# Kernel tuning notes

Measured on AMD Instinct MI355X. Metric: run time of the kernel, lower is better.

## Reference

```python
import jax, jax.numpy as jnp
import numpy as np

N = 1048576
BINS = 32
HID = 64
OUT = 64
IN_DIMS = 7


def setup_inputs() -> dict:
    key = jax.random.key(0)
    ks = jax.random.split(key, 9)
    pos01 = jax.random.uniform(ks[0], (N, 3), dtype=jnp.float32)
    wi01 = jax.random.uniform(ks[1], (N, 3), dtype=jnp.float32)
    rough01 = jax.random.uniform(ks[2], (N, 1), dtype=jnp.float32)
    enc_dim = IN_DIMS * BINS  # 224
    W1 = jax.random.normal(ks[3], (enc_dim, HID), dtype=jnp.float32) / np.sqrt(enc_dim)
    b1 = jnp.zeros((HID,), dtype=jnp.float32)
    W2 = jax.random.normal(ks[4], (HID, HID), dtype=jnp.float32) / np.sqrt(HID)
    b2 = jnp.zeros((HID,), dtype=jnp.float32)
    W3 = jax.random.normal(ks[5], (HID, OUT), dtype=jnp.float32) / np.sqrt(HID)
    b3 = jnp.zeros((OUT,), dtype=jnp.float32)
    centers = jnp.linspace(0.0, 1.0, BINS, dtype=jnp.float32)
    return {"pos01": pos01, "wi01": wi01, "rough01": rough01,
            "W1": W1, "b1": b1, "W2": W2, "b2": b2, "W3": W3, "b3": b3,
            "centers": centers}


def reference(pos01, wi01, rough01, W1, b1, W2, b2, W3, b3, centers):
    # Concatenate + clamp to [0,1]: [N, 7]
    x = jnp.clip(jnp.concatenate([pos01, wi01, rough01], axis=1), 0.0, 1.0)
    sigma = 1.0 / BINS
    # OneBlob gaussian encoding: [N, 7, BINS] -> [N, 7*BINS]
    diff = x[:, :, None] - centers[None, None, :]
    enc = jnp.exp(-0.5 * (diff / sigma) ** 2).reshape(x.shape[0], -1)
    # 3-layer MLP with ReLU
    h = jax.nn.relu(enc @ W1 + b1)
    h = jax.nn.relu(h @ W2 + b2)
    return h @ W3 + b3
```

## Files before the change

kernel.cpp:

```cpp
#include <hip/hip_runtime.h>

typedef __bf16 bf16x8 __attribute__((ext_vector_type(8)));
typedef float  f32x4  __attribute__((ext_vector_type(4)));

constexpr int HID = 64;
constexpr float K1   = 27.178297f;
constexpr float STEP = -K1 / 31.0f;


__global__ void prep_kernel(const float* __restrict__ W1,
                            const float* __restrict__ W2,
                            const float* __restrict__ W3,
                            bf16x8* __restrict__ ws)
{
    const int f = blockIdx.x;
    const int l = threadIdx.x;
    const int g = l >> 4, r = l & 15;
    bf16x8 v;
    if (f < 28) {
        const int kk = f >> 2, mt = f & 3;
#pragma unroll
        for (int j = 0; j < 8; ++j)
            v[j] = (__bf16)W1[(32 * kk + 8 * g + j) * HID + 16 * mt + r];
    } else {
        const float* W = (f < 36) ? W2 : W3;
        const int fi = (f < 36) ? (f - 28) : (f - 36);
        const int mt = fi >> 1, kk2 = fi & 1;
#pragma unroll
        for (int j = 0; j < 8; ++j) {
            const int k = 32 * kk2 + 16 * (j >> 2) + 4 * g + (j & 3);
            v[j] = (__bf16)W[k * HID + 16 * mt + r];
        }
    }
    ws[f * 64 + l] = v;
}

__device__ __forceinline__ void load_x(const float* __restrict__ pos,
                                       const float* __restrict__ wi,
                                       const float* __restrict__ rough,
                                       int row, float* x)
{
    x[0] = pos[row * 3 + 0]; x[1] = pos[row * 3 + 1]; x[2] = pos[row * 3 + 2];
    x[3] = wi[row * 3 + 0];  x[4] = wi[row * 3 + 1];  x[5] = wi[row * 3 + 2];
    x[6] = rough[row];
}

__global__ __launch_bounds__(256, 3)
void cond_net_kernel(const float* __restrict__ pos, const float* __restrict__ wi,
                     const float* __restrict__ rough,
                     const float* __restrict__ b1, const float* __restrict__ b2,
                     const float* __restrict__ b3,
                     const bf16x8* __restrict__ ws,
                     float* __restrict__ out)
{
    __shared__ __align__(16) char lds[44 * 1024 + 768];

    const int tid = threadIdx.x;
    const int l = tid & 63, wv = tid >> 6, g = l >> 4, r = l & 15;

#pragma unroll
    for (int i = 0; i < 11; ++i) {
        const int fr = wv * 11 + i;
        __builtin_amdgcn_global_load_lds(
            (const __attribute__((address_space(1))) void*)(ws + fr * 64 + l),
            (__attribute__((address_space(3))) void*)(lds + fr * 1024),
            16, 0, 0);
    }
    if (wv < 3) {
        const float* bp = (wv == 0) ? b1 : (wv == 1) ? b2 : b3;
        __builtin_amdgcn_global_load_lds(
            (const __attribute__((address_space(1))) void*)(bp + l),
            (__attribute__((address_space(3))) void*)(lds + 44 * 1024 + wv * 256),
            4, 0, 0);
    }

    const int rbase = blockIdx.x * 256 + wv * 64 + r;
    float A[4][7];
#pragma unroll
    for (int t = 0; t < 4; ++t) {
        float x[7];
        load_x(pos, wi, rough, rbase + 16 * t, x);
#pragma unroll
        for (int d = 0; d < 7; ++d)
            A[t][d] = fmaf(K1, fminf(fmaxf(x[d], 0.0f), 1.0f), STEP * (float)(8 * g));
    }

    __syncthreads();

    const char* lb = (const char*)lds + l * 16;
    const char* bb = (const char*)lds + 44 * 1024 + g * 16;

    f32x4 acc1[4][4];
    {
        f32x4 b1v[4];
#pragma unroll
        for (int mt = 0; mt < 4; ++mt) b1v[mt] = *(const f32x4*)(bb + mt * 64);
#pragma unroll
        for (int t = 0; t < 4; ++t)
#pragma unroll
            for (int mt = 0; mt < 4; ++mt) acc1[t][mt] = b1v[mt];
    }

#pragma unroll
    for (int kk = 0; kk < 7; ++kk) {
        bf16x8 e[4];
#pragma unroll
        for (int t = 0; t < 4; ++t)
#pragma unroll
            for (int j = 0; j < 8; ++j) {
                const float d = A[t][kk] + (float)j * STEP;
                e[t][j] = (__bf16)__builtin_amdgcn_exp2f(-(d * d));
            }
#pragma unroll
        for (int mt = 0; mt < 4; ++mt) {
            const bf16x8 wf = *(const bf16x8*)(lb + (kk * 4 + mt) * 1024);
#pragma unroll
            for (int t = 0; t < 4; ++t)
                acc1[t][mt] = __builtin_amdgcn_mfma_f32_16x16x32_bf16(wf, e[t], acc1[t][mt], 0, 0, 0);
        }
    }

#pragma unroll
    for (int p = 0; p < 2; ++p) {
        bf16x8 h1f[2][2];
#pragma unroll
        for (int tt = 0; tt < 2; ++tt)
#pragma unroll
            for (int kk2 = 0; kk2 < 2; ++kk2) {
                bf16x8 v;
#pragma unroll
                for (int j = 0; j < 8; ++j)
                    v[j] = (__bf16)fmaxf(acc1[2 * p + tt][2 * kk2 + (j >> 2)][j & 3], 0.0f);
                h1f[tt][kk2] = v;
            }

        f32x4 acc2[2][4];
#pragma unroll
        for (int mt = 0; mt < 4; ++mt) {
            const f32x4 b2v = *(const f32x4*)(bb + 256 + mt * 64);
            acc2[0][mt] = b2v; acc2[1][mt] = b2v;
        }
#pragma unroll
        for (int kk2 = 0; kk2 < 2; ++kk2)
#pragma unroll
            for (int mt = 0; mt < 4; ++mt) {
                const bf16x8 wf = *(const bf16x8*)(lb + (28 + mt * 2 + kk2) * 1024);
#pragma unroll
                for (int tt = 0; tt < 2; ++tt)
                    acc2[tt][mt] = __builtin_amdgcn_mfma_f32_16x16x32_bf16(wf, h1f[tt][kk2], acc2[tt][mt], 0, 0, 0);
            }

        bf16x8 h2f[2][2];
#pragma unroll
        for (int tt = 0; tt < 2; ++tt)
#pragma unroll
            for (int kk2 = 0; kk2 < 2; ++kk2) {
                bf16x8 v;
#pragma unroll
                for (int j = 0; j < 8; ++j)
                    v[j] = (__bf16)fmaxf(acc2[tt][2 * kk2 + (j >> 2)][j & 3], 0.0f);
                h2f[tt][kk2] = v;
            }

        f32x4 acc3[2][4];
#pragma unroll
        for (int mt = 0; mt < 4; ++mt) {
            const f32x4 b3v = *(const f32x4*)(bb + 512 + mt * 64);
            acc3[0][mt] = b3v; acc3[1][mt] = b3v;
        }
#pragma unroll
        for (int kk2 = 0; kk2 < 2; ++kk2)
#pragma unroll
            for (int mt = 0; mt < 4; ++mt) {
                const bf16x8 wf = *(const bf16x8*)(lb + (36 + mt * 2 + kk2) * 1024);
#pragma unroll
                for (int tt = 0; tt < 2; ++tt)
                    acc3[tt][mt] = __builtin_amdgcn_mfma_f32_16x16x32_bf16(wf, h2f[tt][kk2], acc3[tt][mt], 0, 0, 0);
            }

#pragma unroll
        for (int tt = 0; tt < 2; ++tt) {
            const int row = rbase + 16 * (2 * p + tt);
#pragma unroll
            for (int mt = 0; mt < 4; ++mt)
                __builtin_nontemporal_store(acc3[tt][mt],
                    (f32x4*)(out + (size_t)row * 64 + 16 * mt + 4 * g));
        }
    }
}

extern "C" void kernel_launch(void* const* d_in, const int* in_sizes, int n_in,
                              void* d_out, int out_size, void* d_ws, size_t ws_size,
                              hipStream_t stream) {
    const float* pos     = (const float*)d_in[0];
    const float* wi      = (const float*)d_in[1];
    const float* rough   = (const float*)d_in[2];
    const float* W1      = (const float*)d_in[3];
    const float* b1      = (const float*)d_in[4];
    const float* W2      = (const float*)d_in[5];
    const float* b2      = (const float*)d_in[6];
    const float* W3      = (const float*)d_in[7];
    const float* b3      = (const float*)d_in[8];
    float* out = (float*)d_out;

    bf16x8* ws = (bf16x8*)d_ws;

    const int n = in_sizes[0] / 3;
    hipLaunchKernelGGL(prep_kernel, dim3(44), dim3(64), 0, stream, W1, W2, W3, ws);
    hipLaunchKernelGGL(cond_net_kernel, dim3(n / 256), dim3(256), 0, stream,
                       pos, wi, rough, b1, b2, b3, (const bf16x8*)ws, out);
}
```

Measured before the change: 90.23 us.

## Use 512-thread blocks processing 1024 rows in a loop to amortize weight staging

Blocks grow to 512 threads (8 waves) and each wave runs two iterations of 64 rows, so one block covers 1024 rows and the LDS weight load is amortized over four times as many rows. Layers 2 and 3 now process all four row tiles at once instead of in two halves, and input loads move inside the loop. The risks are higher register pressure from the wider acc2/acc3 arrays under launch_bounds(512,4), and fewer blocks in the grid.

After: 92.76 us. 2.8% more time.

```diff
diff --git a/kernel.cpp b/kernel.cpp
--- a/kernel.cpp
+++ b/kernel.cpp
@@ -45,7 +45,7 @@
     x[6] = rough[row];
 }
 
-__global__ __launch_bounds__(256, 3)
+__global__ __launch_bounds__(512, 4)
 void cond_net_kernel(const float* __restrict__ pos, const float* __restrict__ wi,
                      const float* __restrict__ rough,
                      const float* __restrict__ b1, const float* __restrict__ b2,
@@ -58,14 +58,11 @@
     const int tid = threadIdx.x;
     const int l = tid & 63, wv = tid >> 6, g = l >> 4, r = l & 15;
 
-#pragma unroll
-    for (int i = 0; i < 11; ++i) {
-        const int fr = wv * 11 + i;
+    for (int fr = wv; fr < 44; fr += 8)
         __builtin_amdgcn_global_load_lds(
             (const __attribute__((address_space(1))) void*)(ws + fr * 64 + l),
             (__attribute__((address_space(3))) void*)(lds + fr * 1024),
             16, 0, 0);
-    }
     if (wv < 3) {
         const float* bp = (wv == 0) ? b1 : (wv == 1) ? b2 : b3;
         __builtin_amdgcn_global_load_lds(
@@ -74,71 +71,75 @@
             4, 0, 0);
     }
 
-    const int rbase = blockIdx.x * 256 + wv * 64 + r;
-    float A[4][7];
-#pragma unroll
-    for (int t = 0; t < 4; ++t) {
-        float x[7];
-        load_x(pos, wi, rough, rbase + 16 * t, x);
-#pragma unroll
-        for (int d = 0; d < 7; ++d)
-            A[t][d] = fmaf(K1, fminf(fmaxf(x[d], 0.0f), 1.0f), STEP * (float)(8 * g));
-    }
+    const float base_g = STEP * (float)(8 * g);
+    const int rbase = blockIdx.x * 1024 + wv * 64 + r;
 
     __syncthreads();
 
-    const char* lb = (const char*)lds + l * 16;
-    const char* bb = (const char*)lds + 44 * 1024 + g * 16;
-
-    f32x4 acc1[4][4];
-    {
-        f32x4 b1v[4];
-#pragma unroll
-        for (int mt = 0; mt < 4; ++mt) b1v[mt] = *(const f32x4*)(bb + mt * 64);
+    unsigned int ldsoff = 0;
+#pragma unroll 1
+    for (int it = 0; it < 2; ++it) {
+        asm volatile("" : "+v"(ldsoff));
+        const char* lb = (const char*)lds + ldsoff + l * 16;
+        const char* bb = (const char*)lds + ldsoff + 44 * 1024 + g * 16;
+
+        const int row0 = rbase + it * 512;
+
+        float A[4][7];
+#pragma unroll
+        for (int t = 0; t < 4; ++t) {
+            float x[7];
+            load_x(pos, wi, rough, row0 + 16 * t, x);
+#pragma unroll
+            for (int d = 0; d < 7; ++d)
+                A[t][d] = fmaf(K1, fminf(fmaxf(x[d], 0.0f), 1.0f), base_g);
+        }
+
+        f32x4 acc1[4][4];
+#pragma unroll
+        for (int mt = 0; mt < 4; ++mt) {
+            const f32x4 bv = *(const f32x4*)(bb + mt * 64);
+#pragma unroll
+            for (int t = 0; t < 4; ++t) acc1[t][mt] = bv;
+        }
+
+#pragma unroll
+        for (int kk = 0; kk < 7; ++kk) {
+            bf16x8 e[4];
+#pragma unroll
+            for (int t = 0; t < 4; ++t)
+#pragma unroll
+                for (int j = 0; j < 8; ++j) {
+                    const float d = A[t][kk] + (float)j * STEP;
+                    e[t][j] = (__bf16)__builtin_amdgcn_exp2f(-(d * d));
+                }
+#pragma unroll
+            for (int mt = 0; mt < 4; ++mt) {
+                const bf16x8 wf = *(const bf16x8*)(lb + (kk * 4 + mt) * 1024);
+#pragma unroll
+                for (int t = 0; t < 4; ++t)
+                    acc1[t][mt] = __builtin_amdgcn_mfma_f32_16x16x32_bf16(wf, e[t], acc1[t][mt], 0, 0, 0);
+            }
+        }
+
+        bf16x8 h1f[4][2];
 #pragma unroll
         for (int t = 0; t < 4; ++t)
-#pragma unroll
-            for (int mt = 0; mt < 4; ++mt) acc1[t][mt] = b1v[mt];
-    }
-
-#pragma unroll
-    for (int kk = 0; kk < 7; ++kk) {
-        bf16x8 e[4];
-#pragma unroll
-        for (int t = 0; t < 4; ++t)
-#pragma unroll
-            for (int j = 0; j < 8; ++j) {
-                const float d = A[t][kk] + (float)j * STEP;
-                e[t][j] = (__bf16)__builtin_amdgcn_exp2f(-(d * d));
-            }
-#pragma unroll
-        for (int mt = 0; mt < 4; ++mt) {
-            const bf16x8 wf = *(const bf16x8*)(lb + (kk * 4 + mt) * 1024);
-#pragma unroll
-            for (int t = 0; t < 4; ++t)
-                acc1[t][mt] = __builtin_amdgcn_mfma_f32_16x16x32_bf16(wf, e[t], acc1[t][mt], 0, 0, 0);
-        }
-    }
-
-#pragma unroll
-    for (int p = 0; p < 2; ++p) {
-        bf16x8 h1f[2][2];
-#pragma unroll
-        for (int tt = 0; tt < 2; ++tt)
 #pragma unroll
             for (int kk2 = 0; kk2 < 2; ++kk2) {
                 bf16x8 v;
 #pragma unroll
                 for (int j = 0; j < 8; ++j)
-                    v[j] = (__bf16)fmaxf(acc1[2 * p + tt][2 * kk2 + (j >> 2)][j & 3], 0.0f);
-                h1f[tt][kk2] = v;
-            }
-
-        f32x4 acc2[2][4];
+                    v[j] = (__bf16)fmaxf(acc1[t][2 * kk2 + (j >> 2)][j & 3], 0.0f);
+                h1f[t][kk2] = v;
+            }
+
+        f32x4 acc2[4][4];
 #pragma unroll
         for (int mt = 0; mt < 4; ++mt) {
-            const f32x4 b2v = *(const f32x4*)(bb + 256 + mt * 64);
-            acc2[0][mt] = b2v; acc2[1][mt] = b2v;
+            const f32x4 bv = *(const f32x4*)(bb + 256 + mt * 64);
+#pragma unroll
+            for (int t = 0; t < 4; ++t) acc2[t][mt] = bv;
         }
 #pragma unroll
         for (int kk2 = 0; kk2 < 2; ++kk2)
@@ -146,27 +147,28 @@
             for (int mt = 0; mt < 4; ++mt) {
                 const bf16x8 wf = *(const bf16x8*)(lb + (28 + mt * 2 + kk2) * 1024);
 #pragma unroll
-                for (int tt = 0; tt < 2; ++tt)
-                    acc2[tt][mt] = __builtin_amdgcn_mfma_f32_16x16x32_bf16(wf, h1f[tt][kk2], acc2[tt][mt], 0, 0, 0);
-            }
-
-        bf16x8 h2f[2][2];
-#pragma unroll
-        for (int tt = 0; tt < 2; ++tt)
+                for (int t = 0; t < 4; ++t)
+                    acc2[t][mt] = __builtin_amdgcn_mfma_f32_16x16x32_bf16(wf, h1f[t][kk2], acc2[t][mt], 0, 0, 0);
+            }
+
+        bf16x8 h2f[4][2];
+#pragma unroll
+        for (int t = 0; t < 4; ++t)
 #pragma unroll
             for (int kk2 = 0; kk2 < 2; ++kk2) {
                 bf16x8 v;
 #pragma unroll
                 for (int j = 0; j < 8; ++j)
-                    v[j] = (__bf16)fmaxf(acc2[tt][2 * kk2 + (j >> 2)][j & 3], 0.0f);
-                h2f[tt][kk2] = v;
-            }
-
-        f32x4 acc3[2][4];
+                    v[j] = (__bf16)fmaxf(acc2[t][2 * kk2 + (j >> 2)][j & 3], 0.0f);
+                h2f[t][kk2] = v;
+            }
+
+        f32x4 acc3[4][4];
 #pragma unroll
         for (int mt = 0; mt < 4; ++mt) {
-            const f32x4 b3v = *(const f32x4*)(bb + 512 + mt * 64);
-            acc3[0][mt] = b3v; acc3[1][mt] = b3v;
+            const f32x4 bv = *(const f32x4*)(bb + 512 + mt * 64);
+#pragma unroll
+            for (int t = 0; t < 4; ++t) acc3[t][mt] = bv;
         }
 #pragma unroll
         for (int kk2 = 0; kk2 < 2; ++kk2)
@@ -174,16 +176,16 @@
             for (int mt = 0; mt < 4; ++mt) {
                 const bf16x8 wf = *(const bf16x8*)(lb + (36 + mt * 2 + kk2) * 1024);
 #pragma unroll
-                for (int tt = 0; tt < 2; ++tt)
-                    acc3[tt][mt] = __builtin_amdgcn_mfma_f32_16x16x32_bf16(wf, h2f[tt][kk2], acc3[tt][mt], 0, 0, 0);
-            }
-
-#pragma unroll
-        for (int tt = 0; tt < 2; ++tt) {
-            const int row = rbase + 16 * (2 * p + tt);
+                for (int t = 0; t < 4; ++t)
+                    acc3[t][mt] = __builtin_amdgcn_mfma_f32_16x16x32_bf16(wf, h2f[t][kk2], acc3[t][mt], 0, 0, 0);
+            }
+
+#pragma unroll
+        for (int t = 0; t < 4; ++t) {
+            const int row = row0 + 16 * t;
 #pragma unroll
             for (int mt = 0; mt < 4; ++mt)
-                __builtin_nontemporal_store(acc3[tt][mt],
+                __builtin_nontemporal_store(acc3[t][mt],
                     (f32x4*)(out + (size_t)row * 64 + 16 * mt + 4 * g));
         }
     }
@@ -207,6 +209,6 @@
 
     const int n = in_sizes[0] / 3;
     hipLaunchKernelGGL(prep_kernel, dim3(44), dim3(64), 0, stream, W1, W2, W3, ws);
-    hipLaunchKernelGGL(cond_net_kernel, dim3(n / 256), dim3(256), 0, stream,
+    hipLaunchKernelGGL(cond_net_kernel, dim3(n / 1024), dim3(512), 0, stream,
                        pos, wi, rough, b1, b2, b3, (const bf16x8*)ws, out);
 }
```
